# Kernel optimization log

Measured on AMD Instinct MI355X. Metric: run time of the kernel, lower is better.

The kernel has to match this reference:

```python
import jax, jax.numpy as jnp
import numpy as np

N_V = 100000   # vertices
N_E = 20000    # hyperedges
N_PAIRS = 1600000  # incidence pairs
F = 128
H = 128
EPS = 1e-5


def setup_inputs() -> dict:
    key = jax.random.key(0)
    k1, k2, k3, k4 = jax.random.split(key, 4)
    X = jax.random.normal(k1, (N_V, F), dtype=jnp.float32)
    vertex_ids = jax.random.randint(k2, (N_PAIRS,), 0, N_V, dtype=jnp.int32)
    edge_ids = jax.random.randint(k3, (N_PAIRS,), 0, N_E, dtype=jnp.int32)
    W = jax.random.normal(k4, (F, H), dtype=jnp.float32) * (1.0 / np.sqrt(F))
    b = jnp.zeros((H,), dtype=jnp.float32)
    gamma = jnp.ones((H,), dtype=jnp.float32)
    beta = jnp.zeros((H,), dtype=jnp.float32)
    return {"X": X, "vertex_ids": vertex_ids, "edge_ids": edge_ids,
            "W": W, "b": b, "gamma": gamma, "beta": beta}


def _segment_mean(vals, ids, num_segments):
    s = jax.ops.segment_sum(vals, ids, num_segments=num_segments)
    cnt = jax.ops.segment_sum(jnp.ones((ids.shape[0], 1), vals.dtype), ids,
                              num_segments=num_segments)
    return s / jnp.maximum(cnt, 1.0)


def reference(X, vertex_ids, edge_ids, W, b, gamma, beta):
    # linear: theta
    h = X @ W + b                                    # [N_V, H]
    # batchnorm (batch statistics, as in training mode)
    mu = jnp.mean(h, axis=0)
    var = jnp.var(h, axis=0)
    h = (h - mu) * jax.lax.rsqrt(var + EPS) * gamma + beta
    # hypergraph v2v mean: vertex -> hyperedge mean, then hyperedge -> vertex mean
    Xe = _segment_mean(h[vertex_ids], edge_ids, N_E)   # [N_E, H]
    Xv = _segment_mean(Xe[edge_ids], vertex_ids, N_V)  # [N_V, H]
    # activation (ReLU); dropout is identity in eval
    return jax.nn.relu(Xv)
```

## Files before the change

kernel.cpp:

```cpp
#include <hip/hip_runtime.h>
#include <hip/hip_bf16.h>

#define N_V 100000
#define N_E 20000
#define N_P 1600000
#define FDIM 128
#define HDIM 128
#define BN_EPS 1e-5f

#define SORT_C 4096
#define SORT_BLOCKS ((N_P + SORT_C - 1) / SORT_C)
#define NB_E 313
#define EB_SHIFT 6
#define EB_REGION 9216
#define EB_SORT 5888
#define NB_V 391
#define VB_SHIFT 8
#define VB_REGION 8192
#define VB_SORT 4608
#define SENTINEL 0xFFFFFFFFu

#define EIDX_CAP 192
#define VIDX_CAP 64

#define GEMM_BLOCKS 625
#define WT_STRIDE 136
#define BN_BLOCKS 400
#define BN_RPB 250

typedef __attribute__((ext_vector_type(8))) short short8;
typedef __attribute__((ext_vector_type(4))) float floatx4;

__device__ __forceinline__ float bf_lo(unsigned u) {
    return __uint_as_float(u << 16);
}
__device__ __forceinline__ float bf_hi(unsigned u) {
    return __uint_as_float(u & 0xffff0000u);
}
__device__ __forceinline__ unsigned short f2bf(float f) {
    unsigned u = __float_as_uint(f);
    return (unsigned short)((u + 0x7fffu + ((u >> 16) & 1u)) >> 16);
}

__device__ __forceinline__ void acc4(float* s, const uint2& u) {
    s[0] += bf_lo(u.x); s[1] += bf_hi(u.x);
    s[2] += bf_lo(u.y); s[3] += bf_hi(u.y);
}

__device__ __forceinline__ void acc8(float* s, const uint4& u) {
    s[0] += bf_lo(u.x); s[1] += bf_hi(u.x);
    s[2] += bf_lo(u.y); s[3] += bf_hi(u.y);
    s[4] += bf_lo(u.z); s[5] += bf_hi(u.z);
    s[6] += bf_lo(u.w); s[7] += bf_hi(u.w);
}

union SmemGemmSort {
    struct {
        unsigned short WTs[FDIM * WT_STRIDE];
    } g;
    struct {
        unsigned stageE[SORT_C];
        unsigned stageV[SORT_C];
        int histE[NB_E], curE[NB_E], offsE[NB_E], gbaseE[NB_E];
        int histV[NB_V], curV[NB_V], offsV[NB_V], gbaseV[NB_V];
        int partial[256];
    } s;
};

union SmemBnCsr {
    struct {
        unsigned B[EB_SORT];
        int hist[256];
        int offs[257];
        int cur[256];
    } c;
    struct {
        float ls[128], lss[128];
    } b;
};

__device__ void gemm_body(int bid, unsigned short* WTs,
                          const float* __restrict__ X,
                          const float* __restrict__ W,
                          const float* __restrict__ bias,
                          unsigned* __restrict__ h_u) {
    const int t = threadIdx.x;
    for (int idx = t; idx < FDIM * HDIM; idx += 256) {
        const int k = idx >> 7, m = idx & 127;
        WTs[m * WT_STRIDE + k] = f2bf(W[idx]);
    }
    __syncthreads();

    const int wave = t >> 6, lane = t & 63;
    const int quad = lane >> 4, sub = lane & 15;
    const int nstrips = N_V / 16;

    for (int s = bid * 4 + wave; s < nstrips; s += GEMM_BLOCKS * 4) {
        const int row0 = s * 16;
        short8 xf[4];
        const float* xp = X + (size_t)(row0 + sub) * FDIM + quad * 8;
        #pragma unroll
        for (int kt = 0; kt < 4; ++kt) {
            const float4 a = *(const float4*)(xp + kt * 32);
            const float4 b2 = *(const float4*)(xp + kt * 32 + 4);
            short8 f;
            f[0] = (short)f2bf(a.x);  f[1] = (short)f2bf(a.y);
            f[2] = (short)f2bf(a.z);  f[3] = (short)f2bf(a.w);
            f[4] = (short)f2bf(b2.x); f[5] = (short)f2bf(b2.y);
            f[6] = (short)f2bf(b2.z); f[7] = (short)f2bf(b2.w);
            xf[kt] = f;
        }
        #pragma unroll
        for (int tile = 0; tile < 8; ++tile) {
            floatx4 acc = {0.f, 0.f, 0.f, 0.f};
            const unsigned short* wp =
                WTs + (tile * 16 + sub) * WT_STRIDE + quad * 8;
            #pragma unroll
            for (int kt = 0; kt < 4; ++kt) {
                const short8 af = *(const short8*)(wp + kt * 32);
                acc = __builtin_amdgcn_mfma_f32_16x16x32_bf16(af, xf[kt], acc,
                                                              0, 0, 0);
            }
            const int ch = tile * 16 + quad * 4;
            const float4 bb = *(const float4*)(bias + ch);
            const float c0 = acc[0] + bb.x, c1 = acc[1] + bb.y;
            const float c2 = acc[2] + bb.z, c3 = acc[3] + bb.w;
            const unsigned lo = (unsigned)f2bf(c0) | ((unsigned)f2bf(c1) << 16);
            const unsigned hi = (unsigned)f2bf(c2) | ((unsigned)f2bf(c3) << 16);
            uint2* dst = (uint2*)(h_u + (size_t)(row0 + sub) * 64 + (ch >> 1));
            *dst = make_uint2(lo, hi);
        }
    }
}

__device__ void sort_body(int bid, SmemGemmSort* sm,
                          const int* __restrict__ vid,
                          const int* __restrict__ eid,
                          int* __restrict__ gcntE, int* __restrict__ gcntV,
                          unsigned* __restrict__ partE,
                          unsigned* __restrict__ partV) {
    unsigned* stageE = sm->s.stageE;
    unsigned* stageV = sm->s.stageV;
    int* histE = sm->s.histE; int* curE = sm->s.curE;
    int* offsE = sm->s.offsE; int* gbaseE = sm->s.gbaseE;
    int* histV = sm->s.histV; int* curV = sm->s.curV;
    int* offsV = sm->s.offsV; int* gbaseV = sm->s.gbaseV;
    int* partial = sm->s.partial;
    const int t = threadIdx.x;
    const int p0 = bid * SORT_C;
    const int n = min(SORT_C, N_P - p0);
    const int n4 = n >> 2;
    const int4* e4p = (const int4*)(eid + p0);
    const int4* v4p = (const int4*)(vid + p0);

    for (int k = t; k < NB_E; k += 256) histE[k] = 0;
    for (int k = t; k < NB_V; k += 256) histV[k] = 0;
    __syncthreads();
    for (int i = t; i < n4; i += 256) {
        const int4 e4 = e4p[i];
        const int4 v4 = v4p[i];
        atomicAdd(&histE[((unsigned)e4.x) >> EB_SHIFT], 1);
        atomicAdd(&histE[((unsigned)e4.y) >> EB_SHIFT], 1);
        atomicAdd(&histE[((unsigned)e4.z) >> EB_SHIFT], 1);
        atomicAdd(&histE[((unsigned)e4.w) >> EB_SHIFT], 1);
        atomicAdd(&histV[((unsigned)v4.x) >> VB_SHIFT], 1);
        atomicAdd(&histV[((unsigned)v4.y) >> VB_SHIFT], 1);
        atomicAdd(&histV[((unsigned)v4.z) >> VB_SHIFT], 1);
        atomicAdd(&histV[((unsigned)v4.w) >> VB_SHIFT], 1);
    }
    __syncthreads();
    {
        constexpr int G = (NB_E + 255) / 256;
        int loc[G]; int s = 0;
        #pragma unroll
        for (int g = 0; g < G; ++g) {
            int idx = t * G + g; loc[g] = s;
            if (idx < NB_E) s += histE[idx];
        }
        partial[t] = s;
        __syncthreads();
        for (int d = 1; d < 256; d <<= 1) {
            int x = (t >= d) ? partial[t - d] : 0;
            __syncthreads(); partial[t] += x; __syncthreads();
        }
        const int base = t ? partial[t - 1] : 0;
        #pragma unroll
        for (int g = 0; g < G; ++g) {
            int idx = t * G + g;
            if (idx < NB_E) { offsE[idx] = base + loc[g]; curE[idx] = base + loc[g]; }
        }
        __syncthreads();
    }
    {
        constexpr int G = (NB_V + 255) / 256;
        int loc[G]; int s = 0;
        #pragma unroll
        for (int g = 0; g < G; ++g) {
            int idx = t * G + g; loc[g] = s;
            if (idx < NB_V) s += histV[idx];
        }
        partial[t] = s;
        __syncthreads();
        for (int d = 1; d < 256; d <<= 1) {
            int x = (t >= d) ? partial[t - d] : 0;
            __syncthreads(); partial[t] += x; __syncthreads();
        }
        const int base = t ? partial[t - 1] : 0;
        #pragma unroll
        for (int g = 0; g < G; ++g) {
            int idx = t * G + g;
            if (idx < NB_V) { offsV[idx] = base + loc[g]; curV[idx] = base + loc[g]; }
        }
        __syncthreads();
    }
    for (int i = t; i < n4; i += 256) {
        const int4 e4 = e4p[i];
        const int4 v4 = v4p[i];
        #pragma unroll
        for (int q = 0; q < 4; ++q) {
            const int ev = (q == 0) ? e4.x : (q == 1) ? e4.y : (q == 2) ? e4.z : e4.w;
            const int vv = (q == 0) ? v4.x : (q == 1) ? v4.y : (q == 2) ? v4.z : v4.w;
            const unsigned pkE = ((unsigned)(ev & 63) << 17) | (unsigned)vv;
            stageE[atomicAdd(&curE[(unsigned)ev >> EB_SHIFT], 1)] = pkE;
            const unsigned pkV = ((unsigned)(vv & 255) << 15) | (unsigned)ev;
            stageV[atomicAdd(&curV[(unsigned)vv >> VB_SHIFT], 1)] = pkV;
        }
    }
    __syncthreads();
    for (int k = t; k < NB_E; k += 256) {
        const int c = histE[k];
        gbaseE[k] = c ? atomicAdd(&gcntE[k], (c + 15) & ~15) : 0;
    }
    for (int k = t; k < NB_V; k += 256) {
        const int c = histV[k];
        gbaseV[k] = c ? atomicAdd(&gcntV[k], (c + 15) & ~15) : 0;
    }
    __syncthreads();
    for (int k = t >> 3; k < NB_E; k += 32) {
        const int c = histE[k];
        if (c == 0) continue;
        int cpad = (c + 15) & ~15;
        const int gb = gbaseE[k];
        if (gb >= EB_REGION) continue;
        cpad = min(cpad, EB_REGION - gb);
        unsigned* dst = partE + (size_t)k * EB_REGION + gb;
        const int lo = offsE[k];
        for (int j = (t & 7) * 4; j + 3 < cpad; j += 32) {
            uint4 w;
            w.x = (j + 0 < c) ? stageE[lo + j + 0] : SENTINEL;
            w.y = (j + 1 < c) ? stageE[lo + j + 1] : SENTINEL;
            w.z = (j + 2 < c) ? stageE[lo + j + 2] : SENTINEL;
            w.w = (j + 3 < c) ? stageE[lo + j + 3] : SENTINEL;
            *(uint4*)(dst + j) = w;
        }
    }
    for (int k = t >> 3; k < NB_V; k += 32) {
        const int c = histV[k];
        if (c == 0) continue;
        int cpad = (c + 15) & ~15;
        const int gb = gbaseV[k];
        if (gb >= VB_REGION) continue;
        cpad = min(cpad, VB_REGION - gb);
        unsigned* dst = partV + (size_t)k * VB_REGION + gb;
        const int lo = offsV[k];
        for (int j = (t & 7) * 4; j + 3 < cpad; j += 32) {
            uint4 w;
            w.x = (j + 0 < c) ? stageV[lo + j + 0] : SENTINEL;
            w.y = (j + 1 < c) ? stageV[lo + j + 1] : SENTINEL;
            w.z = (j + 2 < c) ? stageV[lo + j + 2] : SENTINEL;
            w.w = (j + 3 < c) ? stageV[lo + j + 3] : SENTINEL;
            *(uint4*)(dst + j) = w;
        }
    }
}

__global__ __launch_bounds__(256) void k_gemm_sort(
    const float* __restrict__ X, const float* __restrict__ W,
    const float* __restrict__ bias, unsigned* __restrict__ h_u,
    const int* __restrict__ vid, const int* __restrict__ eid,
    int* __restrict__ gcntE, int* __restrict__ gcntV,
    unsigned* __restrict__ partE, unsigned* __restrict__ partV) {
    __shared__ __align__(16) SmemGemmSort sm;
    const int b = blockIdx.x;
    if (b < GEMM_BLOCKS)
        gemm_body(b, sm.g.WTs, X, W, bias, h_u);
    else
        sort_body(b - GEMM_BLOCKS, &sm, vid, eid, gcntE, gcntV, partE, partV);
}

__device__ void bn_body(int bid, float* ls, float* lss,
                        const unsigned* __restrict__ h_u,
                        float* __restrict__ sums) {
    const int t = threadIdx.x;
    const int c8 = t & 15;
    const int rw = t >> 4;
    const int r0 = bid * BN_RPB;
    const int r1 = min(r0 + BN_RPB, N_V);
    float s[8] = {0.f,0.f,0.f,0.f,0.f,0.f,0.f,0.f};
    float ss[8] = {0.f,0.f,0.f,0.f,0.f,0.f,0.f,0.f};
    for (int r = r0 + rw; r < r1; r += 16) {
        const uint4 u = *(const uint4*)(h_u + (size_t)r * 64 + c8 * 4);
        const float x0 = bf_lo(u.x), x1 = bf_hi(u.x);
        const float x2 = bf_lo(u.y), x3 = bf_hi(u.y);
        const float x4 = bf_lo(u.z), x5 = bf_hi(u.z);
        const float x6 = bf_lo(u.w), x7 = bf_hi(u.w);
        s[0]+=x0; ss[0]+=x0*x0;  s[1]+=x1; ss[1]+=x1*x1;
        s[2]+=x2; ss[2]+=x2*x2;  s[3]+=x3; ss[3]+=x3*x3;
        s[4]+=x4; ss[4]+=x4*x4;  s[5]+=x5; ss[5]+=x5*x5;
        s[6]+=x6; ss[6]+=x6*x6;  s[7]+=x7; ss[7]+=x7*x7;
    }
    #pragma unroll
    for (int k = 0; k < 8; ++k) {
        s[k]  += __shfl_xor(s[k], 16);  s[k]  += __shfl_xor(s[k], 32);
        ss[k] += __shfl_xor(ss[k], 16); ss[k] += __shfl_xor(ss[k], 32);
    }
    for (int k = t; k < 128; k += 256) { ls[k] = 0.f; lss[k] = 0.f; }
    __syncthreads();
    if ((t & 63) < 16) {
        #pragma unroll
        for (int k = 0; k < 8; ++k) {
            atomicAdd(&ls[c8 * 8 + k], s[k]);
            atomicAdd(&lss[c8 * 8 + k], ss[k]);
        }
    }
    __syncthreads();
    if (t < 128) {
        atomicAdd(&sums[t],       ls[t]);
        atomicAdd(&sums[128 + t], lss[t]);
    }
}

template <int NKEY, int PACK_SHIFT, int CAP, int REGION, int STRIDE>
__device__ void csr_body(int bkt, const unsigned* __restrict__ part,
                         const int* __restrict__ gcnt, int nkeys_total,
                         int* __restrict__ segoff, int* __restrict__ segcnt,
                         unsigned* __restrict__ csr,
                         unsigned* B, int* hist, int* offs, int* cur) {
    const int t = threadIdx.x;
    const unsigned mask = (1u << PACK_SHIFT) - 1u;
    const int tot = min(gcnt[bkt], REGION);
    const int tot4 = tot >> 2;
    const unsigned* src = part + (size_t)bkt * REGION;

    for (int k = t; k < NKEY; k += 256) { hist[k] = 0; cur[k] = 0; }
    __syncthreads();
    for (int i = t; i < tot4; i += 256) {
        const uint4 a = ((const uint4*)src)[i];
        if (a.x != SENTINEL) atomicAdd(&hist[a.x >> PACK_SHIFT], 1);
        if (a.y != SENTINEL) atomicAdd(&hist[a.y >> PACK_SHIFT], 1);
        if (a.z != SENTINEL) atomicAdd(&hist[a.z >> PACK_SHIFT], 1);
        if (a.w != SENTINEL) atomicAdd(&hist[a.w >> PACK_SHIFT], 1);
    }
    for (int i = tot4 * 4 + t; i < tot; i += 256) {
        const unsigned a = src[i];
        if (a != SENTINEL) atomicAdd(&hist[a >> PACK_SHIFT], 1);
    }
    __syncthreads();
    if (t == 0) {
        int acc = 0;
        for (int k = 0; k < NKEY; ++k) { offs[k] = acc; acc += hist[k]; }
        offs[NKEY] = acc;
    }
    __syncthreads();
    for (int i = t; i < tot4; i += 256) {
        const uint4 a = ((const uint4*)src)[i];
        #pragma unroll
        for (int q = 0; q < 4; ++q) {
            const unsigned av = (q == 0) ? a.x : (q == 1) ? a.y : (q == 2) ? a.z : a.w;
            if (av != SENTINEL) {
                const int k = av >> PACK_SHIFT;
                const int pos = offs[k] + atomicAdd(&cur[k], 1);
                if (pos < CAP) B[pos] = av & mask;
            }
        }
    }
    for (int i = tot4 * 4 + t; i < tot; i += 256) {
        const unsigned av = src[i];
        if (av != SENTINEL) {
            const int k = av >> PACK_SHIFT;
            const int pos = offs[k] + atomicAdd(&cur[k], 1);
            if (pos < CAP) B[pos] = av & mask;
        }
    }
    __syncthreads();
    const int total = min(offs[NKEY], CAP);
    unsigned* dst = csr + (size_t)bkt * STRIDE;
    for (int i = t * 4; i + 3 < total; i += 1024)
        *(uint4*)(dst + i) = *(const uint4*)(&B[i]);
    for (int i = (total & ~3) + t; i < total; i += 256) dst[i] = B[i];
    for (int k = t; k < NKEY; k += 256) {
        const int g = bkt * NKEY + k;
        if (g < nkeys_total) {
            const int o0 = min(offs[k], CAP);
            const int o1 = min(offs[k + 1], CAP);
            segoff[g] = bkt * STRIDE + o0;
            segcnt[g] = o1 - o0;
        }
    }
}

__global__ __launch_bounds__(256) void k_bn_csr(
    const unsigned* __restrict__ h_u, float* __restrict__ sums,
    const unsigned* __restrict__ partE, const int* __restrict__ gcntE,
    int* __restrict__ eoff, int* __restrict__ ecnt, unsigned* __restrict__ csrE,
    const unsigned* __restrict__ partV, const int* __restrict__ gcntV,
    int* __restrict__ voff, int* __restrict__ vcnt, unsigned* __restrict__ csrV) {
    __shared__ __align__(16) SmemBnCsr sm;
    const int b = blockIdx.x;
    if (b < BN_BLOCKS) {
        bn_body(b, sm.b.ls, sm.b.lss, h_u, sums);
    } else if (b < BN_BLOCKS + NB_E) {
        csr_body<64, 17, EB_SORT, EB_REGION, EB_SORT>(
            b - BN_BLOCKS, partE, gcntE, N_E, eoff, ecnt, csrE,
            sm.c.B, sm.c.hist, sm.c.offs, sm.c.cur);
    } else {
        csr_body<256, 15, VB_SORT, VB_REGION, VB_SORT>(
            b - BN_BLOCKS - NB_E, partV, gcntV, N_V, voff, vcnt, csrV,
            sm.c.B, sm.c.hist, sm.c.offs, sm.c.cur);
    }
}

__global__ void k_bn_final(const float* __restrict__ sums,
                           const float* __restrict__ gamma,
                           const float* __restrict__ beta,
                           float* __restrict__ scale, float* __restrict__ shift) {
    const int c = threadIdx.x;
    const float inv_n = 1.0f / (float)N_V;
    const float mu  = sums[c] * inv_n;
    const float var = sums[128 + c] * inv_n - mu * mu;
    const float inv = rsqrtf(var + BN_EPS);
    const float sc  = gamma[c] * inv;
    scale[c] = sc;
    shift[c] = beta[c] - mu * sc;
}

__global__ __launch_bounds__(256) void k_edge_gather(
    const unsigned* __restrict__ h_u, const unsigned* __restrict__ csrE,
    const int* __restrict__ eoff, const int* __restrict__ ecnt,
    const float* __restrict__ scale, const float* __restrict__ shift,
    unsigned* __restrict__ xe_u) {
    __shared__ int ib[4][EIDX_CAP];
    const int b = blockIdx.x;
    const int xcd = b & 7;
    const int half = xcd >> 2;
    const int grp = (b >> 3) * 4 + (xcd & 3);
    const int wave = threadIdx.x >> 6;
    const int e = grp * 4 + wave;
    const int l = threadIdx.x & 63;
    const int rg = l >> 4, c = l & 15;
    const int wbase = half * 32 + 2 * c;
    int o = 0, n = 0;
    if (e < N_E) { o = eoff[e]; n = ecnt[e]; }
    const int nc = min(n, EIDX_CAP);
    int* mi = ib[wave];
    for (int i = l; i < nc; i += 64) mi[i] = (int)csrE[o + i];
    __syncthreads();

    float s[4] = {0.f, 0.f, 0.f, 0.f};
    int j = 0;
    for (; j + 31 < nc; j += 32) {
        const int r0 = mi[j + rg],      r1 = mi[j + 4 + rg];
        const int r2 = mi[j + 8 + rg],  r3 = mi[j + 12 + rg];
        const int r4 = mi[j + 16 + rg], r5 = mi[j + 20 + rg];
        const int r6 = mi[j + 24 + rg], r7 = mi[j + 28 + rg];
        const uint2 u0 = *(const uint2*)(h_u + (size_t)r0 * 64 + wbase);
        const uint2 u1 = *(const uint2*)(h_u + (size_t)r1 * 64 + wbase);
        const uint2 u2 = *(const uint2*)(h_u + (size_t)r2 * 64 + wbase);
        const uint2 u3 = *(const uint2*)(h_u + (size_t)r3 * 64 + wbase);
        const uint2 u4 = *(const uint2*)(h_u + (size_t)r4 * 64 + wbase);
        const uint2 u5 = *(const uint2*)(h_u + (size_t)r5 * 64 + wbase);
        const uint2 u6 = *(const uint2*)(h_u + (size_t)r6 * 64 + wbase);
        const uint2 u7 = *(const uint2*)(h_u + (size_t)r7 * 64 + wbase);
        acc4(s, u0); acc4(s, u1); acc4(s, u2); acc4(s, u3);
        acc4(s, u4); acc4(s, u5); acc4(s, u6); acc4(s, u7);
    }
    for (; j + 15 < nc; j += 16) {
        const int r0 = mi[j + rg],     r1 = mi[j + 4 + rg];
        const int r2 = mi[j + 8 + rg], r3 = mi[j + 12 + rg];
        const uint2 u0 = *(const uint2*)(h_u + (size_t)r0 * 64 + wbase);
        const uint2 u1 = *(const uint2*)(h_u + (size_t)r1 * 64 + wbase);
        const uint2 u2 = *(const uint2*)(h_u + (size_t)r2 * 64 + wbase);
        const uint2 u3 = *(const uint2*)(h_u + (size_t)r3 * 64 + wbase);
        acc4(s, u0); acc4(s, u1); acc4(s, u2); acc4(s, u3);
    }
    for (; j < nc; j += 4) {
        if (j + rg < nc) {
            const int r = mi[j + rg];
            const uint2 u = *(const uint2*)(h_u + (size_t)r * 64 + wbase);
            acc4(s, u);
        }
    }
    for (int jj = nc; jj < n; jj += 4) {
        if (jj + rg < n) {
            const int r = (int)csrE[o + jj + rg];
            const uint2 u = *(const uint2*)(h_u + (size_t)r * 64 + wbase);
            acc4(s, u);
        }
    }
    #pragma unroll
    for (int k = 0; k < 4; ++k) {
        s[k] += __shfl_xor(s[k], 16);
        s[k] += __shfl_xor(s[k], 32);
    }
    if (e < N_E && rg == 0) {
        float m[4] = {0.f, 0.f, 0.f, 0.f};
        if (n > 0) {
            const float rc = 1.0f / (float)n;
            const float4 sc4 = ((const float4*)scale)[half * 16 + c];
            const float4 sh4 = ((const float4*)shift)[half * 16 + c];
            m[0] = sc4.x * s[0] * rc + sh4.x;
            m[1] = sc4.y * s[1] * rc + sh4.y;
            m[2] = sc4.z * s[2] * rc + sh4.z;
            m[3] = sc4.w * s[3] * rc + sh4.w;
        }
        uint2 pk;
        pk.x = (unsigned)f2bf(m[0]) | ((unsigned)f2bf(m[1]) << 16);
        pk.y = (unsigned)f2bf(m[2]) | ((unsigned)f2bf(m[3]) << 16);
        *(uint2*)(xe_u + (size_t)e * 64 + wbase) = pk;
    }
}

__global__ __launch_bounds__(256) void k_vert_gather(
    const unsigned* __restrict__ xe_u, const unsigned* __restrict__ csrV,
    const int* __restrict__ voff, const int* __restrict__ vcnt,
    float* __restrict__ out) {
    __shared__ int ib[4][VIDX_CAP];
    const int wave = threadIdx.x >> 6;
    const int v = blockIdx.x * 4 + wave;
    const int l = threadIdx.x & 63;
    const int g = l >> 4, c = l & 15;
    int o = 0, n = 0;
    if (v < N_V) { o = voff[v]; n = vcnt[v]; }
    const int nc = min(n, VIDX_CAP);
    int* mi = ib[wave];
    for (int i = l; i < nc; i += 64) mi[i] = (int)csrV[o + i];
    __syncthreads();

    float s[8] = {0.f, 0.f, 0.f, 0.f, 0.f, 0.f, 0.f, 0.f};
    int j = 0;
    for (; j + 15 < nc; j += 16) {
        const int r0 = mi[j + g],     r1 = mi[j + 4 + g];
        const int r2 = mi[j + 8 + g], r3 = mi[j + 12 + g];
        const uint4 u0 = *(const uint4*)(xe_u + (size_t)r0 * 64 + 4 * c);
        const uint4 u1 = *(const uint4*)(xe_u + (size_t)r1 * 64 + 4 * c);
        const uint4 u2 = *(const uint4*)(xe_u + (size_t)r2 * 64 + 4 * c);
        const uint4 u3 = *(const uint4*)(xe_u + (size_t)r3 * 64 + 4 * c);
        acc8(s, u0); acc8(s, u1); acc8(s, u2); acc8(s, u3);
    }
    for (; j < nc; j += 4) {
        if (j + g < nc) {
            const int r = mi[j + g];
            const uint4 u = *(const uint4*)(xe_u + (size_t)r * 64 + 4 * c);
            acc8(s, u);
        }
    }
    for (int jj = nc; jj < n; jj += 4) {
        if (jj + g < n) {
            const int r = (int)csrV[o + jj + g];
            const uint4 u = *(const uint4*)(xe_u + (size_t)r * 64 + 4 * c);
            acc8(s, u);
        }
    }
    #pragma unroll
    for (int k = 0; k < 8; ++k) {
        s[k] += __shfl_xor(s[k], 16);
        s[k] += __shfl_xor(s[k], 32);
    }
    if (v < N_V && g == 0) {
        const float rc = 1.0f / (float)max(n, 1);
        float4 r0, r1;
        r0.x = fmaxf(s[0] * rc, 0.f);
        r0.y = fmaxf(s[1] * rc, 0.f);
        r0.z = fmaxf(s[2] * rc, 0.f);
        r0.w = fmaxf(s[3] * rc, 0.f);
        r1.x = fmaxf(s[4] * rc, 0.f);
        r1.y = fmaxf(s[5] * rc, 0.f);
        r1.z = fmaxf(s[6] * rc, 0.f);
        r1.w = fmaxf(s[7] * rc, 0.f);
        ((float4*)out)[(size_t)v * 32 + 2 * c]     = r0;
        ((float4*)out)[(size_t)v * 32 + 2 * c + 1] = r1;
    }
}

extern "C" void kernel_launch(void* const* d_in, const int* in_sizes, int n_in,
                              void* d_out, int out_size, void* d_ws, size_t ws_size,
                              hipStream_t stream) {
    const float* X     = (const float*)d_in[0];
    const int*   vid   = (const int*)d_in[1];
    const int*   eid   = (const int*)d_in[2];
    const float* W     = (const float*)d_in[3];
    const float* b     = (const float*)d_in[4];
    const float* gamma = (const float*)d_in[5];
    const float* beta  = (const float*)d_in[6];
    float* out = (float*)d_out;

    char* ws = (char*)d_ws;
    unsigned* h_u   = (unsigned*)ws;  ws += (size_t)N_V * 64 * 4;
    unsigned* xe_u  = (unsigned*)ws;  ws += (size_t)N_E * 64 * 4;
    unsigned* partE = (unsigned*)ws;  ws += (size_t)NB_E * EB_REGION * 4;
    unsigned* partV = (unsigned*)ws;  ws += (size_t)NB_V * VB_REGION * 4;
    unsigned* csrE  = (unsigned*)ws;  ws += (size_t)NB_E * EB_SORT * 4;
    unsigned* csrV  = (unsigned*)ws;  ws += (size_t)NB_V * VB_SORT * 4;
    int* eoff = (int*)ws;             ws += (size_t)N_E * 4;
    int* ecnt = (int*)ws;             ws += (size_t)N_E * 4;
    int* voff = (int*)ws;             ws += (size_t)N_V * 4;
    int* vcnt = (int*)ws;             ws += (size_t)N_V * 4;
    char* zbase = ws;
    int*   gcntE = (int*)ws;          ws += (size_t)NB_E * 4;
    int*   gcntV = (int*)ws;          ws += (size_t)NB_V * 4;
    float* sums  = (float*)ws;        ws += 256 * 4;
    float* scale = (float*)ws;        ws += 128 * 4;
    float* shift = (float*)ws;        ws += 128 * 4;

    hipMemsetAsync(zbase, 0, (size_t)((char*)scale - zbase), stream);

    k_gemm_sort<<<GEMM_BLOCKS + SORT_BLOCKS, 256, 0, stream>>>(
        X, W, b, h_u, vid, eid, gcntE, gcntV, partE, partV);

    k_bn_csr<<<BN_BLOCKS + NB_E + NB_V, 256, 0, stream>>>(
        h_u, sums, partE, gcntE, eoff, ecnt, csrE,
        partV, gcntV, voff, vcnt, csrV);

    k_bn_final<<<1, 128, 0, stream>>>(sums, gamma, beta, scale, shift);

    k_edge_gather<<<(N_E / 4) * 2, 256, 0, stream>>>(h_u, csrE, eoff, ecnt,
                                                     scale, shift, xe_u);
    k_vert_gather<<<(N_V + 3) / 4, 256, 0, stream>>>(xe_u, csrV, voff, vcnt,
                                                     out);
}
```

Baseline: 259.2 us.

## Split sort blocks per direction and fold BN finalize into edge gather

Each sort block used to bin both the edge-keyed and vertex-keyed partitions. That work is now split into two separate sets of blocks, one per direction, which doubles the sort grid, shrinks shared memory per block and lets more blocks run at once. The tiny single-block BN-finalize kernel is removed. The edge gather now computes the scale and shift from the raw sums inline, which saves a launch but repeats the rsqrt math in every output lane.

Result: no change. 262.0 us (+1.1%).

```diff
diff --git a/kernel.cpp b/kernel.cpp
--- a/kernel.cpp
+++ b/kernel.cpp
@@ -54,17 +54,20 @@
     s[6] += bf_lo(u.w); s[7] += bf_hi(u.w);
 }
 
-union SmemGemmSort {
+union SmemK1 {
     struct {
         unsigned short WTs[FDIM * WT_STRIDE];
     } g;
     struct {
-        unsigned stageE[SORT_C];
-        unsigned stageV[SORT_C];
-        int histE[NB_E], curE[NB_E], offsE[NB_E], gbaseE[NB_E];
-        int histV[NB_V], curV[NB_V], offsV[NB_V], gbaseV[NB_V];
+        unsigned stage[SORT_C];
+        int hist[NB_E], cur[NB_E], offs[NB_E], gbase[NB_E];
         int partial[256];
-    } s;
+    } se;
+    struct {
+        unsigned stage[SORT_C];
+        int hist[NB_V], cur[NB_V], offs[NB_V], gbase[NB_V];
+        int partial[256];
+    } sv;
 };
 
 union SmemBnCsr {
@@ -133,49 +136,37 @@
     }
 }
 
-__device__ void sort_body(int bid, SmemGemmSort* sm,
-                          const int* __restrict__ vid,
-                          const int* __restrict__ eid,
-                          int* __restrict__ gcntE, int* __restrict__ gcntV,
-                          unsigned* __restrict__ partE,
-                          unsigned* __restrict__ partV) {
-    unsigned* stageE = sm->s.stageE;
-    unsigned* stageV = sm->s.stageV;
-    int* histE = sm->s.histE; int* curE = sm->s.curE;
-    int* offsE = sm->s.offsE; int* gbaseE = sm->s.gbaseE;
-    int* histV = sm->s.histV; int* curV = sm->s.curV;
-    int* offsV = sm->s.offsV; int* gbaseV = sm->s.gbaseV;
-    int* partial = sm->s.partial;
+template <int NB, int BSHIFT, int REGION, bool EDGE>
+__device__ void sort_dir_body(int bid, unsigned* stage, int* hist, int* cur,
+                              int* offs, int* gbase, int* partial,
+                              const int* __restrict__ keys,
+                              const int* __restrict__ vals,
+                              int* __restrict__ gcnt,
+                              unsigned* __restrict__ part) {
     const int t = threadIdx.x;
     const int p0 = bid * SORT_C;
     const int n = min(SORT_C, N_P - p0);
     const int n4 = n >> 2;
-    const int4* e4p = (const int4*)(eid + p0);
-    const int4* v4p = (const int4*)(vid + p0);
-
-    for (int k = t; k < NB_E; k += 256) histE[k] = 0;
-    for (int k = t; k < NB_V; k += 256) histV[k] = 0;
+    const int4* k4p = (const int4*)(keys + p0);
+    const int4* v4p = (const int4*)(vals + p0);
+
+    for (int k = t; k < NB; k += 256) hist[k] = 0;
     __syncthreads();
     for (int i = t; i < n4; i += 256) {
-        const int4 e4 = e4p[i];
-        const int4 v4 = v4p[i];
-        atomicAdd(&histE[((unsigned)e4.x) >> EB_SHIFT], 1);
-        atomicAdd(&histE[((unsigned)e4.y) >> EB_SHIFT], 1);
-        atomicAdd(&histE[((unsigned)e4.z) >> EB_SHIFT], 1);
-        atomicAdd(&histE[((unsigned)e4.w) >> EB_SHIFT], 1);
-        atomicAdd(&histV[((unsigned)v4.x) >> VB_SHIFT], 1);
-        atomicAdd(&histV[((unsigned)v4.y) >> VB_SHIFT], 1);
-        atomicAdd(&histV[((unsigned)v4.z) >> VB_SHIFT], 1);
-        atomicAdd(&histV[((unsigned)v4.w) >> VB_SHIFT], 1);
+        const int4 k4 = k4p[i];
+        atomicAdd(&hist[((unsigned)k4.x) >> BSHIFT], 1);
+        atomicAdd(&hist[((unsigned)k4.y) >> BSHIFT], 1);
+        atomicAdd(&hist[((unsigned)k4.z) >> BSHIFT], 1);
+        atomicAdd(&hist[((unsigned)k4.w) >> BSHIFT], 1);
     }
     __syncthreads();
     {
-        constexpr int G = (NB_E + 255) / 256;
+        constexpr int G = (NB + 255) / 256;
         int loc[G]; int s = 0;
         #pragma unroll
         for (int g = 0; g < G; ++g) {
             int idx = t * G + g; loc[g] = s;
-            if (idx < NB_E) s += histE[idx];
+            if (idx < NB) s += hist[idx];
         }
         partial[t] = s;
         __syncthreads();
@@ -187,88 +178,44 @@
         #pragma unroll
         for (int g = 0; g < G; ++g) {
             int idx = t * G + g;
-            if (idx < NB_E) { offsE[idx] = base + loc[g]; curE[idx] = base + loc[g]; }
+            if (idx < NB) { offs[idx] = base + loc[g]; cur[idx] = base + loc[g]; }
         }
         __syncthreads();
     }
-    {
-        constexpr int G = (NB_V + 255) / 256;
-        int loc[G]; int s = 0;
-        #pragma unroll
-        for (int g = 0; g < G; ++g) {
-            int idx = t * G + g; loc[g] = s;
-            if (idx < NB_V) s += histV[idx];
-        }
-        partial[t] = s;
-        __syncthreads();
-        for (int d = 1; d < 256; d <<= 1) {
-            int x = (t >= d) ? partial[t - d] : 0;
-            __syncthreads(); partial[t] += x; __syncthreads();
-        }
-        const int base = t ? partial[t - 1] : 0;
-        #pragma unroll
-        for (int g = 0; g < G; ++g) {
-            int idx = t * G + g;
-            if (idx < NB_V) { offsV[idx] = base + loc[g]; curV[idx] = base + loc[g]; }
-        }
-        __syncthreads();
-    }
     for (int i = t; i < n4; i += 256) {
-        const int4 e4 = e4p[i];
+        const int4 k4 = k4p[i];
         const int4 v4 = v4p[i];
         #pragma unroll
         for (int q = 0; q < 4; ++q) {
-            const int ev = (q == 0) ? e4.x : (q == 1) ? e4.y : (q == 2) ? e4.z : e4.w;
+            const int kk = (q == 0) ? k4.x : (q == 1) ? k4.y : (q == 2) ? k4.z : k4.w;
             const int vv = (q == 0) ? v4.x : (q == 1) ? v4.y : (q == 2) ? v4.z : v4.w;
-            const unsigned pkE = ((unsigned)(ev & 63) << 17) | (unsigned)vv;
-            stageE[atomicAdd(&curE[(unsigned)ev >> EB_SHIFT], 1)] = pkE;
-            const unsigned pkV = ((unsigned)(vv & 255) << 15) | (unsigned)ev;
-            stageV[atomicAdd(&curV[(unsigned)vv >> VB_SHIFT], 1)] = pkV;
-        }
-    }
-    __syncthreads();
-    for (int k = t; k < NB_E; k += 256) {
-        const int c = histE[k];
-        gbaseE[k] = c ? atomicAdd(&gcntE[k], (c + 15) & ~15) : 0;
-    }
-    for (int k = t; k < NB_V; k += 256) {
-        const int c = histV[k];
-        gbaseV[k] = c ? atomicAdd(&gcntV[k], (c + 15) & ~15) : 0;
-    }
-    __syncthreads();
-    for (int k = t >> 3; k < NB_E; k += 32) {
-        const int c = histE[k];
+            const unsigned pk = EDGE
+                ? (((unsigned)(kk & 63) << 17) | (unsigned)vv)
+                : (((unsigned)(kk & 255) << 15) | (unsigned)vv);
+            stage[atomicAdd(&cur[(unsigned)kk >> BSHIFT], 1)] = pk;
+        }
+    }
+    __syncthreads();
+    for (int k = t; k < NB; k += 256) {
+        const int c = hist[k];
+        gbase[k] = c ? atomicAdd(&gcnt[k], (c + 15) & ~15) : 0;
+    }
+    __syncthreads();
+    for (int k = t >> 3; k < NB; k += 32) {
+        const int c = hist[k];
         if (c == 0) continue;
         int cpad = (c + 15) & ~15;
-        const int gb = gbaseE[k];
-        if (gb >= EB_REGION) continue;
-        cpad = min(cpad, EB_REGION - gb);
-        unsigned* dst = partE + (size_t)k * EB_REGION + gb;
-        const int lo = offsE[k];
+        const int gb = gbase[k];
+        if (gb >= REGION) continue;
+        cpad = min(cpad, REGION - gb);
+        unsigned* dst = part + (size_t)k * REGION + gb;
+        const int lo = offs[k];
         for (int j = (t & 7) * 4; j + 3 < cpad; j += 32) {
             uint4 w;
-            w.x = (j + 0 < c) ? stageE[lo + j + 0] : SENTINEL;
-            w.y = (j + 1 < c) ? stageE[lo + j + 1] : SENTINEL;
-            w.z = (j + 2 < c) ? stageE[lo + j + 2] : SENTINEL;
-            w.w = (j + 3 < c) ? stageE[lo + j + 3] : SENTINEL;
-            *(uint4*)(dst + j) = w;
-        }
-    }
-    for (int k = t >> 3; k < NB_V; k += 32) {
-        const int c = histV[k];
-        if (c == 0) continue;
-        int cpad = (c + 15) & ~15;
-        const int gb = gbaseV[k];
-        if (gb >= VB_REGION) continue;
-        cpad = min(cpad, VB_REGION - gb);
-        unsigned* dst = partV + (size_t)k * VB_REGION + gb;
-        const int lo = offsV[k];
-        for (int j = (t & 7) * 4; j + 3 < cpad; j += 32) {
-            uint4 w;
-            w.x = (j + 0 < c) ? stageV[lo + j + 0] : SENTINEL;
-            w.y = (j + 1 < c) ? stageV[lo + j + 1] : SENTINEL;
-            w.z = (j + 2 < c) ? stageV[lo + j + 2] : SENTINEL;
-            w.w = (j + 3 < c) ? stageV[lo + j + 3] : SENTINEL;
+            w.x = (j + 0 < c) ? stage[lo + j + 0] : SENTINEL;
+            w.y = (j + 1 < c) ? stage[lo + j + 1] : SENTINEL;
+            w.z = (j + 2 < c) ? stage[lo + j + 2] : SENTINEL;
+            w.w = (j + 3 < c) ? stage[lo + j + 3] : SENTINEL;
             *(uint4*)(dst + j) = w;
         }
     }
@@ -280,12 +227,19 @@
     const int* __restrict__ vid, const int* __restrict__ eid,
     int* __restrict__ gcntE, int* __restrict__ gcntV,
     unsigned* __restrict__ partE, unsigned* __restrict__ partV) {
-    __shared__ __align__(16) SmemGemmSort sm;
+    __shared__ __align__(16) SmemK1 sm;
     const int b = blockIdx.x;
-    if (b < GEMM_BLOCKS)
+    if (b < GEMM_BLOCKS) {
         gemm_body(b, sm.g.WTs, X, W, bias, h_u);
-    else
-        sort_body(b - GEMM_BLOCKS, &sm, vid, eid, gcntE, gcntV, partE, partV);
+    } else if (b < GEMM_BLOCKS + SORT_BLOCKS) {
+        sort_dir_body<NB_E, EB_SHIFT, EB_REGION, true>(
+            b - GEMM_BLOCKS, sm.se.stage, sm.se.hist, sm.se.cur, sm.se.offs,
+            sm.se.gbase, sm.se.partial, eid, vid, gcntE, partE);
+    } else {
+        sort_dir_body<NB_V, VB_SHIFT, VB_REGION, false>(
+            b - GEMM_BLOCKS - SORT_BLOCKS, sm.sv.stage, sm.sv.hist, sm.sv.cur,
+            sm.sv.offs, sm.sv.gbase, sm.sv.partial, vid, eid, gcntV, partV);
+    }
 }
 
 __device__ void bn_body(int bid, float* ls, float* lss,
@@ -420,25 +374,11 @@
     }
 }
 
-__global__ void k_bn_final(const float* __restrict__ sums,
-                           const float* __restrict__ gamma,
-                           const float* __restrict__ beta,
-                           float* __restrict__ scale, float* __restrict__ shift) {
-    const int c = threadIdx.x;
-    const float inv_n = 1.0f / (float)N_V;
-    const float mu  = sums[c] * inv_n;
-    const float var = sums[128 + c] * inv_n - mu * mu;
-    const float inv = rsqrtf(var + BN_EPS);
-    const float sc  = gamma[c] * inv;
-    scale[c] = sc;
-    shift[c] = beta[c] - mu * sc;
-}
-
 __global__ __launch_bounds__(256) void k_edge_gather(
     const unsigned* __restrict__ h_u, const unsigned* __restrict__ csrE,
     const int* __restrict__ eoff, const int* __restrict__ ecnt,
-    const float* __restrict__ scale, const float* __restrict__ shift,
-    unsigned* __restrict__ xe_u) {
+    const float* __restrict__ sums, const float* __restrict__ gamma,
+    const float* __restrict__ beta, unsigned* __restrict__ xe_u) {
     __shared__ int ib[4][EIDX_CAP];
     const int b = blockIdx.x;
     const int xcd = b & 7;
@@ -503,15 +443,22 @@
         s[k] += __shfl_xor(s[k], 32);
     }
     if (e < N_E && rg == 0) {
-        float m[4] = {0.f, 0.f, 0.f, 0.f};
-        if (n > 0) {
-            const float rc = 1.0f / (float)n;
-            const float4 sc4 = ((const float4*)scale)[half * 16 + c];
-            const float4 sh4 = ((const float4*)shift)[half * 16 + c];
-            m[0] = sc4.x * s[0] * rc + sh4.x;
-            m[1] = sc4.y * s[1] * rc + sh4.y;
-            m[2] = sc4.z * s[2] * rc + sh4.z;
-            m[3] = sc4.w * s[3] * rc + sh4.w;
+        const float inv_n = 1.0f / (float)N_V;
+        const float rc = (n > 0) ? (1.0f / (float)n) : 0.f;
+        float m[4];
+        #pragma unroll
+        for (int q = 0; q < 4; ++q) {
+            const int ch = half * 64 + c * 4 + q;
+            float mv = 0.f;
+            if (n > 0) {
+                const float mu  = sums[ch] * inv_n;
+                const float var = sums[128 + ch] * inv_n - mu * mu;
+                const float inv = rsqrtf(var + BN_EPS);
+                const float sc  = gamma[ch] * inv;
+                const float sh  = beta[ch] - mu * sc;
+                mv = sc * s[q] * rc + sh;
+            }
+            m[q] = mv;
         }
         uint2 pk;
         pk.x = (unsigned)f2bf(m[0]) | ((unsigned)f2bf(m[1]) << 16);
@@ -609,22 +556,19 @@
     int*   gcntE = (int*)ws;          ws += (size_t)NB_E * 4;
     int*   gcntV = (int*)ws;          ws += (size_t)NB_V * 4;
     float* sums  = (float*)ws;        ws += 256 * 4;
-    float* scale = (float*)ws;        ws += 128 * 4;
-    float* shift = (float*)ws;        ws += 128 * 4;
-
-    hipMemsetAsync(zbase, 0, (size_t)((char*)scale - zbase), stream);
-
-    k_gemm_sort<<<GEMM_BLOCKS + SORT_BLOCKS, 256, 0, stream>>>(
+    char* zend = ws;
+
+    hipMemsetAsync(zbase, 0, (size_t)(zend - zbase), stream);
+
+    k_gemm_sort<<<GEMM_BLOCKS + 2 * SORT_BLOCKS, 256, 0, stream>>>(
         X, W, b, h_u, vid, eid, gcntE, gcntV, partE, partV);
 
     k_bn_csr<<<BN_BLOCKS + NB_E + NB_V, 256, 0, stream>>>(
         h_u, sums, partE, gcntE, eoff, ecnt, csrE,
         partV, gcntV, voff, vcnt, csrV);
 
-    k_bn_final<<<1, 128, 0, stream>>>(sums, gamma, beta, scale, shift);
-
     k_edge_gather<<<(N_E / 4) * 2, 256, 0, stream>>>(h_u, csrE, eoff, ecnt,
-                                                     scale, shift, xe_u);
+                                                     sums, gamma, beta, xe_u);
     k_vert_gather<<<(N_V + 3) / 4, 256, 0, stream>>>(xe_u, csrV, voff, vcnt,
                                                      out);
 }
```
